# Optimization experiments

Measured on AMD Instinct MI355X. Metric: run time of the kernel, lower is better.

Reference implementation:

```python
import jax, jax.numpy as jnp
import numpy as np

B, S, D, H, R = 16, 2048, 1024, 1024, 16


def setup_inputs() -> dict:
    key = jax.random.key(0)
    ks = jax.random.split(key, 6)
    inv = 1.0 / np.sqrt(D)
    return {
        "x": jax.random.normal(ks[0], (B, S, D), jnp.float32),
        "Wa": jax.random.uniform(ks[1], (H, D), jnp.float32, -inv, inv),
        "ba": jnp.zeros((H,), jnp.float32),
        "Wg": jax.random.uniform(ks[2], (R, D), jnp.float32, -inv, inv),
        "bg": jnp.zeros((R,), jnp.float32),
        "Wu": jax.random.uniform(ks[3], (H, D), jnp.float32, -inv, inv),
        "bu": jnp.zeros((H,), jnp.float32),
        "u": jax.random.normal(ks[4], (H, R), jnp.float32) * 0.02,
        "v": jax.random.normal(ks[5], (H, R), jnp.float32) * 0.02,
    }


def reference(x, Wa, ba, Wg, bg, Wu, bu, u, v):
    # Precompute all per-step projections in big GEMMs (same math as the
    # per-step Linear calls in the original loop).
    a = jax.nn.sigmoid(jnp.einsum('bsd,hd->bsh', x, Wa) + ba)   # [B,S,H]
    g = jnp.einsum('bsd,rd->bsr', x, Wg) + bg                    # [B,S,R]
    u_in = jnp.einsum('bsd,hd->bsh', x, Wu) + bu                 # [B,S,H]

    def step(state, ins):
        a_t, g_t, u_t = ins                      # [B,H], [B,R], [B,H]
        low_rank = (state @ v) * g_t             # [B,R]
        state = a_t * state + u_t + low_rank @ u.T
        return state, None

    init = jnp.zeros((x.shape[0], Wa.shape[0]), x.dtype)
    seq = (jnp.swapaxes(a, 0, 1), jnp.swapaxes(g, 0, 1), jnp.swapaxes(u_in, 0, 1))
    state, _ = jax.lax.scan(step, init, seq)
    return state  # [B, H]
```

## Files before the change

### kernel.cpp

```cpp
#include <hip/hip_runtime.h>
#include <hip/hip_bf16.h>
#include <stdint.h>

#define Bb 16
#define Ss 2048
#define Dd 1024
#define Hh 1024
#define Rr 16
#define Mm 32768

typedef __attribute__((ext_vector_type(4))) float f32x4;
typedef __attribute__((ext_vector_type(8))) short bf16x8;
typedef __attribute__((ext_vector_type(2))) _Float16 h2;

__device__ __forceinline__ unsigned short f2bf(float f) {
    union { float f; uint32_t u; } c; c.f = f;
    uint32_t u = c.u + 0x7fffu + ((c.u >> 16) & 1u);
    return (unsigned short)(u >> 16);
}
__device__ __forceinline__ float bfbits2f(uint32_t bits) {
    union { uint32_t u; float f; } c; c.u = bits << 16; return c.f;
}
__device__ __forceinline__ h2 u2h(unsigned int x) {
    union { unsigned int u; h2 h; } c; c.u = x; return c.h;
}
__device__ __forceinline__ h2 mkh2(float a, float b) {
    h2 r; r.x = (_Float16)a; r.y = (_Float16)b; return r;
}
__device__ __forceinline__ uint32_t h2u(h2 x) {
    union { h2 h; uint32_t u; } c; c.h = x; return c.u;
}

__device__ __forceinline__ float DOT2(h2 a, h2 b, float c) {
#if __has_builtin(__builtin_amdgcn_fdot2)
    return __builtin_amdgcn_fdot2(a, b, c, false);
#else
    return fmaf((float)a.x, (float)b.x, fmaf((float)a.y, (float)b.y, c));
#endif
}

__device__ __forceinline__ float dpp_xor8(float x) {
    return __int_as_float(__builtin_amdgcn_mov_dpp(
        __float_as_int(x), 0x128, 0xF, 0xF, false));
}

__device__ __forceinline__ void gld16(const void* gsrc, void* ldst) {
    __builtin_amdgcn_global_load_lds(
        (const __attribute__((address_space(1))) unsigned int*)gsrc,
        (__attribute__((address_space(3))) unsigned int*)ldst, 16, 0, 0);
}

__device__ __forceinline__ void softbar() {
    __asm volatile("" ::: "memory");
    __builtin_amdgcn_s_waitcnt(0xC07F);
    __builtin_amdgcn_s_barrier();
    __asm volatile("" ::: "memory");
}

__global__ __launch_bounds__(256) void k_convert(
    const float* __restrict__ x, const float* __restrict__ Wa,
    const float* __restrict__ Wu,
    unsigned short* __restrict__ xb, unsigned short* __restrict__ Wab,
    unsigned short* __restrict__ Wub)
{
    long e = ((long)blockIdx.x * 256 + threadIdx.x) * 4;
    const long nx = (long)Mm * Dd;
    const long nw = (long)Hh * Dd;
    const float* src; unsigned short* dst; long o;
    if (e < nx)            { src = x;  dst = xb;  o = e; }
    else if (e < nx + nw)  { src = Wa; dst = Wab; o = e - nx; }
    else                   { src = Wu; dst = Wub; o = e - nx - nw; }
    float4 f = *(const float4*)(src + o);
    ushort4 r;
    r.x = f2bf(f.x); r.y = f2bf(f.y); r.z = f2bf(f.z); r.w = f2bf(f.w);
    *(ushort4*)(dst + o) = r;
}

__global__ __launch_bounds__(256) void k_gemm(
    const unsigned short* __restrict__ Xb,
    const unsigned short* __restrict__ Wab,
    const unsigned short* __restrict__ Wub,
    const float* __restrict__ ba, const float* __restrict__ bu,
    unsigned short* __restrict__ outA, unsigned short* __restrict__ outU)
{
    __shared__ short At[128 * 32];
    __shared__ short Bt[128 * 32];

    const int tid  = threadIdx.x;
    const int lane = tid & 63;
    const int wave = tid >> 6;
    const int bm = blockIdx.x;
    const int bn = blockIdx.y;
    const int region = bn >> 3;
    const int nbase = (bn & 7) * 128;

    const short* Ag = (const short*)Xb;
    const short* Bg = (const short*)(region ? Wub : Wab);
    const float* bias = region ? bu : ba;
    unsigned short* outp = region ? outU : outA;

    const int wm = wave & 1, wn = wave >> 1;
    const int srow = lane >> 2, sseg = lane & 3;
    const int mrow = lane & 15, kb = lane >> 4;

    f32x4 acc[4][4] = {};

    for (int kt = 0; kt < 32; ++kt) {
        __syncthreads();
        const int k0 = kt * 32;
        #pragma unroll
        for (int p = 0; p < 2; ++p) {
            const int row = p * 64 + wave * 16 + srow;
            const short* ga = Ag + (long)(bm * 128 + row) * Dd + k0 + sseg * 8;
            gld16((const void*)ga, (void*)&At[p * 2048 + wave * 512]);
            const short* gb = Bg + (long)(nbase + row) * Dd + k0 + sseg * 8;
            gld16((const void*)gb, (void*)&Bt[p * 2048 + wave * 512]);
        }
        __syncthreads();

        bf16x8 af[4], bq[4];
        #pragma unroll
        for (int i = 0; i < 4; ++i) {
            af[i] = *(const bf16x8*)&At[(wm * 64 + i * 16 + mrow) * 32 + kb * 8];
            bq[i] = *(const bf16x8*)&Bt[(wn * 64 + i * 16 + mrow) * 32 + kb * 8];
        }
        #pragma unroll
        for (int i = 0; i < 4; ++i)
            #pragma unroll
            for (int j = 0; j < 4; ++j)
                acc[i][j] = __builtin_amdgcn_mfma_f32_16x16x32_bf16(
                    af[i], bq[j], acc[i][j], 0, 0, 0);
    }

    const int col = lane & 15, rq = lane >> 4;
    #pragma unroll
    for (int j = 0; j < 4; ++j) {
        const int n = nbase + wn * 64 + j * 16 + col;
        const float bv = bias[n];
        #pragma unroll
        for (int i = 0; i < 4; ++i) {
            const int mb = bm * 128 + wm * 64 + i * 16 + rq * 4;
            #pragma unroll
            for (int r = 0; r < 4; ++r) {
                float vv = acc[i][j][r] + bv;
                if (region == 0) vv = 1.0f / (1.0f + __expf(-vv));
                outp[(long)(mb + r) * Hh + n] = f2bf(vv);
            }
        }
    }
}

__global__ __launch_bounds__(256) void k_g(
    const float* __restrict__ x, const float* __restrict__ Wg,
    const float* __restrict__ bg, float* __restrict__ g)
{
    const int tid = threadIdx.x;
    const int r = tid & 15, ml = tid >> 4;
    const long m = (long)blockIdx.x * 16 + ml;
    const float4* xr = (const float4*)(x + m * Dd);
    const float4* wr = (const float4*)(Wg + (long)r * Dd);
    float acc = 0.0f;
    #pragma unroll 4
    for (int k = 0; k < Dd / 4; ++k) {
        float4 a = xr[k], b = wr[k];
        acc = fmaf(a.x, b.x, acc); acc = fmaf(a.y, b.y, acc);
        acc = fmaf(a.z, b.z, acc); acc = fmaf(a.w, b.w, acc);
    }
    g[m * Rr + r] = acc + bg[r];
}

__global__ __launch_bounds__(256) void k_K(
    const float* __restrict__ u, const float* __restrict__ v,
    float* __restrict__ Kbuf)
{
    const int r = threadIdx.x >> 4;
    const int c = threadIdx.x & 15;
    float acc = 0.0f;
    for (int h = 0; h < Hh; ++h)
        acc = fmaf(v[h * Rr + r], u[h * Rr + c], acc);
    Kbuf[r * 16 + c] = acc;
}

__global__ __launch_bounds__(512) void k_scan(
    const unsigned short* __restrict__ a,
    const unsigned short* __restrict__ uin,
    const float* __restrict__ g,
    const float* __restrict__ u,
    const float* __restrict__ v,
    const float* __restrict__ Kbuf,
    float* __restrict__ out)
{
    __shared__ __align__(16) h2 shad[2][512];
    __shared__ __align__(16) _Float16 cacc[2][16][8];

    const int tid  = threadIdx.x;
    const int lane = tid & 63;
    const int wave = tid >> 6;
    const int oA   = lane >> 3;
    const int pA   = lane & 7;
    const int ra   = lane & 15;
    const int b    = blockIdx.x;
    const int h0   = 2 * tid;

    const int hW = wave * 128 + oA * 16;
    h2 vrA[8], vrB[8];
    #pragma unroll
    for (int k = 0; k < 8; ++k) {
        vrA[k] = mkh2(v[(hW + 2*k) * Rr + pA],
                      v[(hW + 2*k + 1) * Rr + pA]);
        vrB[k] = mkh2(v[(hW + 2*k) * Rr + pA + 8],
                      v[(hW + 2*k + 1) * Rr + pA + 8]);
    }
    h2 ur0[8], ur1[8], kr[8];
    #pragma unroll
    for (int j = 0; j < 8; ++j) {
        ur0[j] = mkh2(u[h0 * Rr + j],        u[h0 * Rr + j + 8]);
        ur1[j] = mkh2(u[(h0 + 1) * Rr + j],  u[(h0 + 1) * Rr + j + 8]);
        kr[j]  = mkh2(Kbuf[ra * 16 + j],     Kbuf[ra * 16 + j + 8]);
    }

    const uint32_t* apu = (const uint32_t*)(a   + (long)b * Ss * Hh) + tid;
    const uint32_t* upu = (const uint32_t*)(uin + (long)b * Ss * Hh) + tid;
    const float*    gp  = g + (long)b * Ss * Rr + ra;

    float s0 = 0.0f, s1 = 0.0f, y = 0.0f;

    uint32_t pa_[4], pu_[4]; float pg_[4];
    pa_[2] = apu[1*512]; pa_[3] = apu[2*512]; pa_[0] = apu[3*512]; pa_[1] = apu[4*512];
    pu_[2] = upu[1*512]; pu_[3] = upu[2*512]; pu_[0] = upu[3*512]; pu_[1] = upu[4*512];
    uint32_t u0r = upu[0];
    apu += 5 * 512; upu += 5 * 512;
    pg_[1] = gp[0]; pg_[2] = gp[Rr]; pg_[3] = gp[2*Rr]; pg_[0] = gp[3*Rr];
    gp += 4 * Rr;

    float tA = bfbits2f(u0r & 0xFFFFu);
    float tB = bfbits2f(u0r >> 16);
    shad[1][tid] = mkh2(tA, tB);
    __syncthreads();

    const h2 one2 = mkh2(1.0f, 1.0f);

#define BODY(RG, RA, PAR, PF) do {                                          \
             \
    uint4 w0 = *(const uint4*)&shad[PAR][wave * 64 + oA * 8];               \
    uint4 w1 = *(const uint4*)&shad[PAR][wave * 64 + oA * 8 + 4];           \
       \
    float q = pg_[RG] * y;                                                  \
    float qo = dpp_xor8(q);                                                 \
    uint32_t qpk = h2u(mkh2(q, qo));                                        \
    uint32_t qv[8];                                                         \
    qv[0] = (uint32_t)__builtin_amdgcn_readlane((int)qpk, 0);               \
    qv[1] = (uint32_t)__builtin_amdgcn_readlane((int)qpk, 1);               \
    qv[2] = (uint32_t)__builtin_amdgcn_readlane((int)qpk, 2);               \
    qv[3] = (uint32_t)__builtin_amdgcn_readlane((int)qpk, 3);               \
    qv[4] = (uint32_t)__builtin_amdgcn_readlane((int)qpk, 4);               \
    qv[5] = (uint32_t)__builtin_amdgcn_readlane((int)qpk, 5);               \
    qv[6] = (uint32_t)__builtin_amdgcn_readlane((int)qpk, 6);               \
    qv[7] = (uint32_t)__builtin_amdgcn_readlane((int)qpk, 7);               \
                                                   \
    float lr0, lr1;                                                         \
    lr0 = DOT2(u2h(qv[0]), ur0[0], 0.0f);                                   \
    lr0 = DOT2(u2h(qv[1]), ur0[1], lr0); lr0 = DOT2(u2h(qv[2]), ur0[2], lr0);\
    lr0 = DOT2(u2h(qv[3]), ur0[3], lr0); lr0 = DOT2(u2h(qv[4]), ur0[4], lr0);\
    lr0 = DOT2(u2h(qv[5]), ur0[5], lr0); lr0 = DOT2(u2h(qv[6]), ur0[6], lr0);\
    lr0 = DOT2(u2h(qv[7]), ur0[7], lr0);                                    \
    lr1 = DOT2(u2h(qv[0]), ur1[0], 0.0f);                                   \
    lr1 = DOT2(u2h(qv[1]), ur1[1], lr1); lr1 = DOT2(u2h(qv[2]), ur1[2], lr1);\
    lr1 = DOT2(u2h(qv[3]), ur1[3], lr1); lr1 = DOT2(u2h(qv[4]), ur1[4], lr1);\
    lr1 = DOT2(u2h(qv[5]), ur1[5], lr1); lr1 = DOT2(u2h(qv[6]), ur1[6], lr1);\
    lr1 = DOT2(u2h(qv[7]), ur1[7], lr1);                                    \
    s0 = tA + lr0; s1 = tB + lr1;                                           \
                             \
    float na0 = bfbits2f(pa_[RA] & 0xFFFFu), na1 = bfbits2f(pa_[RA] >> 16); \
    float nu0 = bfbits2f(pu_[RA] & 0xFFFFu), nu1 = bfbits2f(pu_[RA] >> 16); \
    tA = fmaf(na0, s0, nu0); tB = fmaf(na1, s1, nu1);                       \
    shad[PAR ^ 1][tid] = mkh2(tA, tB);                                      \
    if (PF) { pa_[RA] = *apu; apu += 512; pu_[RA] = *upu; upu += 512;       \
              pg_[RG] = *gp; gp += Rr; }                                    \
                                \
    float lo, hi;                                                           \
    lo = DOT2(u2h(w0.x), vrA[0], 0.0f); lo = DOT2(u2h(w0.y), vrA[1], lo);   \
    lo = DOT2(u2h(w0.z), vrA[2], lo);   lo = DOT2(u2h(w0.w), vrA[3], lo);   \
    lo = DOT2(u2h(w1.x), vrA[4], lo);   lo = DOT2(u2h(w1.y), vrA[5], lo);   \
    lo = DOT2(u2h(w1.z), vrA[6], lo);   lo = DOT2(u2h(w1.w), vrA[7], lo);   \
    hi = DOT2(u2h(w0.x), vrB[0], 0.0f); hi = DOT2(u2h(w0.y), vrB[1], hi);   \
    hi = DOT2(u2h(w0.z), vrB[2], hi);   hi = DOT2(u2h(w0.w), vrB[3], hi);   \
    hi = DOT2(u2h(w1.x), vrB[4], hi);   hi = DOT2(u2h(w1.y), vrB[5], hi);   \
    hi = DOT2(u2h(w1.z), vrB[6], hi);   hi = DOT2(u2h(w1.w), vrB[7], hi);   \
    {                                                                       \
        float tlo = dpp_xor8(lo), thi = dpp_xor8(hi);                       \
        float v1 = (lane & 8) ? (hi + thi) : (lo + tlo);                    \
        v1 += __shfl_xor(v1, 16);                                           \
        v1 += __shfl_xor(v1, 32);                                           \
        if (lane < 16) cacc[PAR][lane][wave] = (_Float16)v1;                \
    }                                                                       \
    softbar();                                      \
                                                 \
    uint4 c4 = *(const uint4*)&cacc[PAR][ra][0];                            \
    float wf;                                                               \
    wf = DOT2(u2h(c4.x), one2, 0.0f); wf = DOT2(u2h(c4.y), one2, wf);       \
    wf = DOT2(u2h(c4.z), one2, wf);   wf = DOT2(u2h(c4.w), one2, wf);       \
    float ky;                                                               \
    ky = DOT2(u2h(qv[0]), kr[0], 0.0f);                                     \
    ky = DOT2(u2h(qv[1]), kr[1], ky); ky = DOT2(u2h(qv[2]), kr[2], ky);     \
    ky = DOT2(u2h(qv[3]), kr[3], ky); ky = DOT2(u2h(qv[4]), kr[4], ky);     \
    ky = DOT2(u2h(qv[5]), kr[5], ky); ky = DOT2(u2h(qv[6]), kr[6], ky);     \
    ky = DOT2(u2h(qv[7]), kr[7], ky);                                       \
    y = wf + ky;                                                            \
} while (0)

    for (int t4 = 0; t4 < 511; ++t4) {
        BODY(1, 2, 1, 1); BODY(2, 3, 0, 1); BODY(3, 0, 1, 1); BODY(0, 1, 0, 1);
    }
    BODY(1, 2, 1, 0); BODY(2, 3, 0, 0); BODY(3, 0, 1, 0); BODY(0, 1, 0, 0);
#undef BODY

    *(float2*)(out + (long)b * Hh + h0) = make_float2(s0, s1);
}

extern "C" void kernel_launch(void* const* d_in, const int* in_sizes, int n_in,
                              void* d_out, int out_size, void* d_ws, size_t ws_size,
                              hipStream_t stream)
{
    const float* x  = (const float*)d_in[0];
    const float* Wa = (const float*)d_in[1];
    const float* ba = (const float*)d_in[2];
    const float* Wg = (const float*)d_in[3];
    const float* bg = (const float*)d_in[4];
    const float* Wu = (const float*)d_in[5];
    const float* bu = (const float*)d_in[6];
    const float* u  = (const float*)d_in[7];
    const float* v  = (const float*)d_in[8];
    float* out = (float*)d_out;

    char* ws = (char*)d_ws;
    unsigned short* xb   = (unsigned short*)(ws);
    unsigned short* Wab  = (unsigned short*)(ws + 67108864);
    unsigned short* Wub  = (unsigned short*)(ws + 69206016);
    unsigned short* abuf = (unsigned short*)(ws + 71303168);
    unsigned short* ubuf = (unsigned short*)(ws + 138412032);
    float*          gbuf = (float*)(ws + 205520896);
    float*          Kbuf = (float*)(ws);

    hipLaunchKernelGGL(k_convert, dim3(34816), dim3(256), 0, stream,
                       x, Wa, Wu, xb, Wab, Wub);
    hipLaunchKernelGGL(k_gemm, dim3(256, 16), dim3(256), 0, stream,
                       xb, Wab, Wub, ba, bu, abuf, ubuf);
    hipLaunchKernelGGL(k_K, dim3(1), dim3(256), 0, stream, u, v, Kbuf);
    hipLaunchKernelGGL(k_g, dim3(2048), dim3(256), 0, stream,
                       x, Wg, bg, gbuf);
    hipLaunchKernelGGL(k_scan, dim3(Bb), dim3(512), 0, stream,
                       abuf, ubuf, gbuf, u, v, Kbuf, out);
}
```

Before: 1.591 ms.

## Double-buffer GEMM LDS tiles and restructure scan step to one barrier

The GEMM now double-buffers its LDS tiles. It issues the next k-tile's async global-to-LDS loads before the MFMAs on the current tile, so each iteration needs one barrier instead of two. The scan loop is reordered so the cross-wave reduction result and the K·q correction are read at the top of the next step. Wave 0 writes the K·q term into an extra cacc slot, which removes the redundant per-lane work and moves the softbar to the end of the step. Dot-product chains are split into two accumulators to shorten dependency latency, and prefetch loads use explicit global address-space pointers. The risks are an ordering or race error in the restructured barrier protocol, and extra LDS use that could affect occupancy.

```diff
diff --git a/kernel.cpp b/kernel.cpp
--- a/kernel.cpp
+++ b/kernel.cpp
@@ -29,6 +29,13 @@
 }
 __device__ __forceinline__ uint32_t h2u(h2 x) {
     union { h2 h; uint32_t u; } c; c.h = x; return c.u;
+}
+
+__device__ __forceinline__ uint32_t gload_u32(const uint32_t* p) {
+    return *(const __attribute__((address_space(1))) uint32_t*)(uintptr_t)p;
+}
+__device__ __forceinline__ float gload_f32(const float* p) {
+    return *(const __attribute__((address_space(1))) float*)(uintptr_t)p;
 }
 
 __device__ __forceinline__ float DOT2(h2 a, h2 b, float c) {
@@ -83,8 +90,8 @@
     const float* __restrict__ ba, const float* __restrict__ bu,
     unsigned short* __restrict__ outA, unsigned short* __restrict__ outU)
 {
-    __shared__ short At[128 * 32];
-    __shared__ short Bt[128 * 32];
+    __shared__ short At[2][128 * 32];
+    __shared__ short Bt[2][128 * 32];
 
     const int tid  = threadIdx.x;
     const int lane = tid & 63;
@@ -105,24 +112,30 @@
 
     f32x4 acc[4][4] = {};
 
+#define STAGE(BUF, KT) do {                                                  \
+    const int k0_ = (KT) * 32;                                               \
+    _Pragma("unroll")                                                        \
+    for (int p = 0; p < 2; ++p) {                                            \
+        const int row_ = p * 64 + wave * 16 + srow;                          \
+        const short* ga_ = Ag + (long)(bm * 128 + row_) * Dd + k0_ + sseg*8; \
+        gld16((const void*)ga_, (void*)&At[BUF][p * 2048 + wave * 512]);     \
+        const short* gb_ = Bg + (long)(nbase + row_) * Dd + k0_ + sseg*8;    \
+        gld16((const void*)gb_, (void*)&Bt[BUF][p * 2048 + wave * 512]);     \
+    }                                                                        \
+} while (0)
+
+    STAGE(0, 0);
+    __syncthreads();
+
+    int cur = 0;
     for (int kt = 0; kt < 32; ++kt) {
-        __syncthreads();
-        const int k0 = kt * 32;
-        #pragma unroll
-        for (int p = 0; p < 2; ++p) {
-            const int row = p * 64 + wave * 16 + srow;
-            const short* ga = Ag + (long)(bm * 128 + row) * Dd + k0 + sseg * 8;
-            gld16((const void*)ga, (void*)&At[p * 2048 + wave * 512]);
-            const short* gb = Bg + (long)(nbase + row) * Dd + k0 + sseg * 8;
-            gld16((const void*)gb, (void*)&Bt[p * 2048 + wave * 512]);
-        }
-        __syncthreads();
+        if (kt < 31) STAGE(cur ^ 1, kt + 1);
 
         bf16x8 af[4], bq[4];
         #pragma unroll
         for (int i = 0; i < 4; ++i) {
-            af[i] = *(const bf16x8*)&At[(wm * 64 + i * 16 + mrow) * 32 + kb * 8];
-            bq[i] = *(const bf16x8*)&Bt[(wn * 64 + i * 16 + mrow) * 32 + kb * 8];
+            af[i] = *(const bf16x8*)&At[cur][(wm*64 + i*16 + mrow)*32 + kb*8];
+            bq[i] = *(const bf16x8*)&Bt[cur][(wn*64 + i*16 + mrow)*32 + kb*8];
         }
         #pragma unroll
         for (int i = 0; i < 4; ++i)
@@ -130,7 +143,11 @@
             for (int j = 0; j < 4; ++j)
                 acc[i][j] = __builtin_amdgcn_mfma_f32_16x16x32_bf16(
                     af[i], bq[j], acc[i][j], 0, 0, 0);
-    }
+
+        __syncthreads();
+        cur ^= 1;
+    }
+#undef STAGE
 
     const int col = lane & 15, rq = lane >> 4;
     #pragma unroll
@@ -191,7 +208,7 @@
     float* __restrict__ out)
 {
     __shared__ __align__(16) h2 shad[2][512];
-    __shared__ __align__(16) _Float16 cacc[2][16][8];
+    __shared__ __align__(16) _Float16 cacc[2][16][24];
 
     const int tid  = threadIdx.x;
     const int lane = tid & 63;
@@ -223,61 +240,74 @@
     const uint32_t* upu = (const uint32_t*)(uin + (long)b * Ss * Hh) + tid;
     const float*    gp  = g + (long)b * Ss * Rr + ra;
 
-    float s0 = 0.0f, s1 = 0.0f, y = 0.0f;
-
     uint32_t pa_[4], pu_[4]; float pg_[4];
-    pa_[2] = apu[1*512]; pa_[3] = apu[2*512]; pa_[0] = apu[3*512]; pa_[1] = apu[4*512];
-    pu_[2] = upu[1*512]; pu_[3] = upu[2*512]; pu_[0] = upu[3*512]; pu_[1] = upu[4*512];
+    pa_[1] = apu[1*512]; pa_[2] = apu[2*512]; pa_[3] = apu[3*512]; pa_[0] = apu[4*512];
+    pu_[1] = upu[1*512]; pu_[2] = upu[2*512]; pu_[3] = upu[3*512]; pu_[0] = upu[4*512];
     uint32_t u0r = upu[0];
     apu += 5 * 512; upu += 5 * 512;
-    pg_[1] = gp[0]; pg_[2] = gp[Rr]; pg_[3] = gp[2*Rr]; pg_[0] = gp[3*Rr];
+    pg_[0] = gp[0]; pg_[1] = gp[Rr]; pg_[2] = gp[2*Rr]; pg_[3] = gp[3*Rr];
     gp += 4 * Rr;
 
     float tA = bfbits2f(u0r & 0xFFFFu);
     float tB = bfbits2f(u0r >> 16);
-    shad[1][tid] = mkh2(tA, tB);
+    shad[0][tid] = mkh2(tA, tB);
+    {
+        uint32_t* cz = (uint32_t*)&cacc[0][0][0];
+        if (tid < 384) cz[tid] = 0u;
+    }
     __syncthreads();
 
+    float s0f = 0.0f, s1f = 0.0f;
     const h2 one2 = mkh2(1.0f, 1.0f);
 
 #define BODY(RG, RA, PAR, PF) do {                                          \
-             \
+                                           \
+    uint4 c4 = *(const uint4*)&cacc[(PAR)^1][ra][0];                        \
+    uint32_t ck = *(const uint32_t*)&cacc[(PAR)^1][ra][8];                  \
     uint4 w0 = *(const uint4*)&shad[PAR][wave * 64 + oA * 8];               \
     uint4 w1 = *(const uint4*)&shad[PAR][wave * 64 + oA * 8 + 4];           \
-       \
+                                              \
+    float wfa = DOT2(u2h(c4.x), one2, 0.0f);                                \
+    float wfb = DOT2(u2h(c4.y), one2, 0.0f);                                \
+    wfa = DOT2(u2h(c4.z), one2, wfa);                                       \
+    wfb = DOT2(u2h(c4.w), one2, wfb);                                       \
+    float y = (wfa + wfb) + (float)(u2h(ck).x);                             \
+                          \
     float q = pg_[RG] * y;                                                  \
     float qo = dpp_xor8(q);                                                 \
     uint32_t qpk = h2u(mkh2(q, qo));                                        \
-    uint32_t qv[8];                                                         \
-    qv[0] = (uint32_t)__builtin_amdgcn_readlane((int)qpk, 0);               \
-    qv[1] = (uint32_t)__builtin_amdgcn_readlane((int)qpk, 1);               \
-    qv[2] = (uint32_t)__builtin_amdgcn_readlane((int)qpk, 2);               \
-    qv[3] = (uint32_t)__builtin_amdgcn_readlane((int)qpk, 3);               \
-    qv[4] = (uint32_t)__builtin_amdgcn_readlane((int)qpk, 4);               \
-    qv[5] = (uint32_t)__builtin_amdgcn_readlane((int)qpk, 5);               \
-    qv[6] = (uint32_t)__builtin_amdgcn_readlane((int)qpk, 6);               \
-    qv[7] = (uint32_t)__builtin_amdgcn_readlane((int)qpk, 7);               \
-                                                   \
-    float lr0, lr1;                                                         \
-    lr0 = DOT2(u2h(qv[0]), ur0[0], 0.0f);                                   \
-    lr0 = DOT2(u2h(qv[1]), ur0[1], lr0); lr0 = DOT2(u2h(qv[2]), ur0[2], lr0);\
-    lr0 = DOT2(u2h(qv[3]), ur0[3], lr0); lr0 = DOT2(u2h(qv[4]), ur0[4], lr0);\
-    lr0 = DOT2(u2h(qv[5]), ur0[5], lr0); lr0 = DOT2(u2h(qv[6]), ur0[6], lr0);\
-    lr0 = DOT2(u2h(qv[7]), ur0[7], lr0);                                    \
-    lr1 = DOT2(u2h(qv[0]), ur1[0], 0.0f);                                   \
-    lr1 = DOT2(u2h(qv[1]), ur1[1], lr1); lr1 = DOT2(u2h(qv[2]), ur1[2], lr1);\
-    lr1 = DOT2(u2h(qv[3]), ur1[3], lr1); lr1 = DOT2(u2h(qv[4]), ur1[4], lr1);\
-    lr1 = DOT2(u2h(qv[5]), ur1[5], lr1); lr1 = DOT2(u2h(qv[6]), ur1[6], lr1);\
-    lr1 = DOT2(u2h(qv[7]), ur1[7], lr1);                                    \
-    s0 = tA + lr0; s1 = tB + lr1;                                           \
-                             \
+    uint32_t qv0 = (uint32_t)__builtin_amdgcn_readlane((int)qpk, 0);        \
+    uint32_t qv1 = (uint32_t)__builtin_amdgcn_readlane((int)qpk, 1);        \
+    uint32_t qv2 = (uint32_t)__builtin_amdgcn_readlane((int)qpk, 2);        \
+    uint32_t qv3 = (uint32_t)__builtin_amdgcn_readlane((int)qpk, 3);        \
+    uint32_t qv4 = (uint32_t)__builtin_amdgcn_readlane((int)qpk, 4);        \
+    uint32_t qv5 = (uint32_t)__builtin_amdgcn_readlane((int)qpk, 5);        \
+    uint32_t qv6 = (uint32_t)__builtin_amdgcn_readlane((int)qpk, 6);        \
+    uint32_t qv7 = (uint32_t)__builtin_amdgcn_readlane((int)qpk, 7);        \
+                              \
+    float l0a = DOT2(u2h(qv0), ur0[0], 0.0f);                               \
+    float l0b = DOT2(u2h(qv4), ur0[4], 0.0f);                               \
+    l0a = DOT2(u2h(qv1), ur0[1], l0a); l0b = DOT2(u2h(qv5), ur0[5], l0b);   \
+    l0a = DOT2(u2h(qv2), ur0[2], l0a); l0b = DOT2(u2h(qv6), ur0[6], l0b);   \
+    l0a = DOT2(u2h(qv3), ur0[3], l0a); l0b = DOT2(u2h(qv7), ur0[7], l0b);   \
+    float l1a = DOT2(u2h(qv0), ur1[0], 0.0f);                               \
+    float l1b = DOT2(u2h(qv4), ur1[4], 0.0f);                               \
+    l1a = DOT2(u2h(qv1), ur1[1], l1a); l1b = DOT2(u2h(qv5), ur1[5], l1b);   \
+    l1a = DOT2(u2h(qv2), ur1[2], l1a); l1b = DOT2(u2h(qv6), ur1[6], l1b);   \
+    l1a = DOT2(u2h(qv3), ur1[3], l1a); l1b = DOT2(u2h(qv7), ur1[7], l1b);   \
+    s0f = tA + (l0a + l0b);                                                 \
+    s1f = tB + (l1a + l1b);                                                 \
+     \
     float na0 = bfbits2f(pa_[RA] & 0xFFFFu), na1 = bfbits2f(pa_[RA] >> 16); \
     float nu0 = bfbits2f(pu_[RA] & 0xFFFFu), nu1 = bfbits2f(pu_[RA] >> 16); \
-    tA = fmaf(na0, s0, nu0); tB = fmaf(na1, s1, nu1);                       \
-    shad[PAR ^ 1][tid] = mkh2(tA, tB);                                      \
-    if (PF) { pa_[RA] = *apu; apu += 512; pu_[RA] = *upu; upu += 512;       \
-              pg_[RG] = *gp; gp += Rr; }                                    \
-                                \
+    tA = fmaf(na0, s0f, nu0); tB = fmaf(na1, s1f, nu1);                     \
+    shad[(PAR) ^ 1][tid] = mkh2(tA, tB);                                    \
+    if (PF) {                                                               \
+        pa_[RA] = gload_u32(apu); apu += 512;                               \
+        pu_[RA] = gload_u32(upu); upu += 512;                               \
+        pg_[RG] = gload_f32(gp);  gp  += Rr;                                \
+    }                                                                       \
+                        \
     float lo, hi;                                                           \
     lo = DOT2(u2h(w0.x), vrA[0], 0.0f); lo = DOT2(u2h(w0.y), vrA[1], lo);   \
     lo = DOT2(u2h(w0.z), vrA[2], lo);   lo = DOT2(u2h(w0.w), vrA[3], lo);   \
@@ -294,28 +324,25 @@
         v1 += __shfl_xor(v1, 32);                                           \
         if (lane < 16) cacc[PAR][lane][wave] = (_Float16)v1;                \
     }                                                                       \
-    softbar();                                      \
-                                                 \
-    uint4 c4 = *(const uint4*)&cacc[PAR][ra][0];                            \
-    float wf;                                                               \
-    wf = DOT2(u2h(c4.x), one2, 0.0f); wf = DOT2(u2h(c4.y), one2, wf);       \
-    wf = DOT2(u2h(c4.z), one2, wf);   wf = DOT2(u2h(c4.w), one2, wf);       \
-    float ky;                                                               \
-    ky = DOT2(u2h(qv[0]), kr[0], 0.0f);                                     \
-    ky = DOT2(u2h(qv[1]), kr[1], ky); ky = DOT2(u2h(qv[2]), kr[2], ky);     \
-    ky = DOT2(u2h(qv[3]), kr[3], ky); ky = DOT2(u2h(qv[4]), kr[4], ky);     \
-    ky = DOT2(u2h(qv[5]), kr[5], ky); ky = DOT2(u2h(qv[6]), kr[6], ky);     \
-    ky = DOT2(u2h(qv[7]), kr[7], ky);                                       \
-    y = wf + ky;                                                            \
+                                     \
+    if (wave == 0 && lane < 16) {                                           \
+        float ka = DOT2(u2h(qv0), kr[0], 0.0f);                             \
+        float kb2 = DOT2(u2h(qv4), kr[4], 0.0f);                            \
+        ka = DOT2(u2h(qv1), kr[1], ka);  kb2 = DOT2(u2h(qv5), kr[5], kb2);  \
+        ka = DOT2(u2h(qv2), kr[2], ka);  kb2 = DOT2(u2h(qv6), kr[6], kb2);  \
+        ka = DOT2(u2h(qv3), kr[3], ka);  kb2 = DOT2(u2h(qv7), kr[7], kb2);  \
+        cacc[PAR][lane][8] = (_Float16)(ka + kb2);                          \
+    }                                                                       \
+    softbar();                                                              \
 } while (0)
 
     for (int t4 = 0; t4 < 511; ++t4) {
-        BODY(1, 2, 1, 1); BODY(2, 3, 0, 1); BODY(3, 0, 1, 1); BODY(0, 1, 0, 1);
-    }
-    BODY(1, 2, 1, 0); BODY(2, 3, 0, 0); BODY(3, 0, 1, 0); BODY(0, 1, 0, 0);
+        BODY(0, 1, 0, 1); BODY(1, 2, 1, 1); BODY(2, 3, 0, 1); BODY(3, 0, 1, 1);
+    }
+    BODY(0, 1, 0, 0); BODY(1, 2, 1, 0); BODY(2, 3, 0, 0); BODY(3, 0, 1, 0);
 #undef BODY
 
-    *(float2*)(out + (long)b * Hh + h0) = make_float2(s0, s1);
+    *(float2*)(out + (long)b * Hh + h0) = make_float2(s0f, s1f);
 }
 
 extern "C" void kernel_launch(void* const* d_in, const int* in_sizes, int n_in,
```

Measured after the change: 1.559 ms. -2.0%, faster.
